# Kernel optimization log

Hardware: AMD Instinct MI355X
Metric: run time of the kernel (lower is better)

## Reference

```python
import jax, jax.numpy as jnp
import numpy as np

H = 128  # hidden width


def _mlp(xy, W0, b0, W1, b1, W2, b2, W3, b3):
    # xy: [..., 2] -> [..., 1], tanh MLP
    h = jnp.tanh(xy @ W0 + b0)
    h = jnp.tanh(h @ W1 + b1)
    h = jnp.tanh(h @ W2 + b2)
    return h @ W3 + b3


def setup_inputs() -> dict:
    key = jax.random.key(0)
    ks = jax.random.split(key, 8)
    n_int, n_bd = 262144, 16384
    inp = {
        "xy_int": jax.random.uniform(ks[0], (n_int, 2), dtype=jnp.float32),
        "f": jax.random.normal(ks[1], (n_int, 1), dtype=jnp.float32),
        "xy_bd": jax.random.uniform(ks[2], (n_bd, 2), dtype=jnp.float32),
        "g": jax.random.normal(ks[3], (n_bd, 1), dtype=jnp.float32),
        # Glorot-ish scaled weights
        "W0": jax.random.normal(ks[4], (2, H), dtype=jnp.float32) / np.sqrt(2.0),
        "b0": jnp.zeros((H,), jnp.float32),
        "W1": jax.random.normal(ks[5], (H, H), dtype=jnp.float32) / np.sqrt(H),
        "b1": jnp.zeros((H,), jnp.float32),
        "W2": jax.random.normal(ks[6], (H, H), dtype=jnp.float32) / np.sqrt(H),
        "b2": jnp.zeros((H,), jnp.float32),
        "W3": jax.random.normal(ks[7], (H, 1), dtype=jnp.float32) / np.sqrt(H),
        "b3": jnp.zeros((1,), jnp.float32),
    }
    return inp


def reference(xy_int, f, xy_bd, g, W0, b0, W1, b1, W2, b2, W3, b3):
    params = (W0, b0, W1, b1, W2, b2, W3, b3)
    n_int = xy_int.shape[0]
    n_bd = xy_bd.shape[0]

    # boundary loss: 0.5/n_bd * ||u(xy_bd) - g||^2
    pred_bd = _mlp(xy_bd, *params)
    diff_bd = pred_bd.reshape(-1) - g.reshape(-1)
    loss_bound = 0.5 / n_bd * jnp.sum(diff_bd * diff_bd)

    # interior PDE residual: u_xx + u_yy (Laplacian) per collocation point
    def u_scalar(p):  # p: [2] -> scalar
        return _mlp(p[None, :], *params)[0, 0]

    def lap_point(p):
        return jnp.trace(jax.hessian(u_scalar)(p))  # 2x2 Hessian trace

    pred_f = jax.vmap(lap_point)(xy_int)  # [n_int]
    diff_f = pred_f.reshape(-1) - f.reshape(-1)
    loss_f = 0.5 / n_int * jnp.sum(diff_f * diff_f)

    return (loss_bound, loss_f)
```

## Files before the change

kernel.cpp:

```cpp
#include <hip/hip_runtime.h>

#define HID 128
#define PTS 32
#define FRAGS_PER_W 2048
#define WS_ELEMS (FRAGS_PER_W * 8)

typedef float v4f  __attribute__((ext_vector_type(4)));
typedef float v16f __attribute__((ext_vector_type(16)));
typedef short s8v  __attribute__((ext_vector_type(8)));

__device__ __forceinline__ unsigned short f2bf(float f) {
    unsigned u = __builtin_bit_cast(unsigned, f);
    u = (u + 0x7FFFu + ((u >> 16) & 1u)) >> 16;
    return (unsigned short)u;
}

#if __has_builtin(__builtin_amdgcn_cvt_pk_bf16_f32)
typedef __bf16 bf16x2 __attribute__((ext_vector_type(2)));
__device__ __forceinline__ unsigned pk2(float f0, float f1) {
    return __builtin_bit_cast(unsigned, __builtin_amdgcn_cvt_pk_bf16_f32(f0, f1));
}
#else
__device__ __forceinline__ unsigned pk2(float f0, float f1) {
    unsigned u0 = __builtin_bit_cast(unsigned, f0);
    unsigned u1 = __builtin_bit_cast(unsigned, f1);
    u0 += 0x7FFFu + ((u0 >> 16) & 1u);
    u1 += 0x7FFFu + ((u1 >> 16) & 1u);
    return __builtin_amdgcn_perm(u1, u0, 0x07060302u);
}
#endif
__device__ __forceinline__ uint2 pk4(const float* f) {
    uint2 h;
    h.x = pk2(f[0], f[1]);
    h.y = pk2(f[2], f[3]);
    return h;
}

__device__ __forceinline__ float fast_tanh(float x) {
#if __has_builtin(__builtin_amdgcn_exp2f)
    float e = __builtin_amdgcn_exp2f(x * 2.885390081777927f);
#else
    float e = __expf(2.0f * x);
#endif
    float r = __builtin_amdgcn_rcpf(e + 1.0f);
    return 1.0f - 2.0f * r;
}

__device__ __forceinline__ void* sb_at(unsigned short* sBh, int row, int colh) {
    return (char*)sBh + (row << 8) + (((colh << 1)) ^ ((row & 15) << 4));
}

__global__ __launch_bounds__(256) void prep_w_kernel(
    const float* __restrict__ W1, const float* __restrict__ W2,
    unsigned short* __restrict__ ws, float* __restrict__ out)
{
    if (blockIdx.x == 0 && threadIdx.x < 2) out[threadIdx.x] = 0.0f;
    const int t = blockIdx.x * 256 + threadIdx.x;
    const int w = t >> 11;
    const int r = t & 2047;
    const int mw = r >> 9;
    const int ks8 = (r >> 6) & 7;
    const int lane = r & 63;
    const int m = mw * 32 + (lane & 31);
    const int kb = ks8 * 16 + (lane >> 5) * 8;
    const float* W = w ? W2 : W1;
    s8v hv;
    #pragma unroll
    for (int i = 0; i < 8; ++i)
        hv[i] = (short)f2bf(W[(kb + i) * HID + m]);
    *(s8v*)&ws[((size_t)w * FRAGS_PER_W + r) * 8] = hv;
}

template <int NC>
__device__ __forceinline__ void run_pinn(
    const float* __restrict__ xy, const float* __restrict__ tgt,
    const float* __restrict__ W0, const float* __restrict__ b0,
    const float* __restrict__ b1, const float* __restrict__ b2,
    const float* __restrict__ W3, const float* __restrict__ b3,
    const unsigned short* __restrict__ ws, float* __restrict__ out_slot,
    float scale, int pbase, unsigned short* sBh, float* sPart)
{
    const int tid  = threadIdx.x;
    const int lane = tid & 63;
    const int mw   = tid >> 6;
    const int l31  = lane & 31;
    const int kh   = lane >> 5;

    s8v wf[8];
    #pragma unroll
    for (int q = 0; q < 8; ++q)
        wf[q] = *(const s8v*)&ws[(size_t)(mw * 512 + q * 64 + lane) * 8];

    {
        const int tj = tid & 31, tp = tid >> 5;
        const int j0 = tj * 4, p0 = tp * 4;
        float wx[4], wy[4], bb[4], m2s2[4];
        #pragma unroll
        for (int jj = 0; jj < 4; ++jj) {
            wx[jj] = W0[j0 + jj];
            wy[jj] = W0[HID + j0 + jj];
            bb[jj] = b0[j0 + jj];
            m2s2[jj] = -2.0f * fmaf(wx[jj], wx[jj], wy[jj] * wy[jj]);
        }
        #pragma unroll
        for (int pp = 0; pp < 4; ++pp) {
            const int p = p0 + pp;
            const float2 t2 = ((const float2*)xy)[pbase + p];
            float chv[NC][4];
            #pragma unroll
            for (int jj = 0; jj < 4; ++jj) {
                float z = fmaf(t2.x, wx[jj], fmaf(t2.y, wy[jj], bb[jj]));
                float a = fast_tanh(z);
                chv[0][jj] = a;
                if (NC == 4) {
                    float t = fmaf(-a, a, 1.0f);
                    chv[1][jj] = t * wx[jj];
                    chv[2][jj] = t * wy[jj];
                    chv[3][jj] = (a * t) * m2s2[jj];
                }
            }
            #pragma unroll
            for (int c = 0; c < NC; ++c)
                *(uint2*)sb_at(sBh, c * 32 + p, j0) = pk4(chv[c]);
        }
    }
    __syncthreads();

    v16f acc[NC];

    #pragma unroll
    for (int L = 0; L < 2; ++L) {
        #pragma unroll
        for (int nt = 0; nt < NC; ++nt) acc[nt] = (v16f)0.0f;

        #pragma unroll
        for (int q = 0; q < 8; ++q) {
            const int koff = q * 16 + kh * 8;
            #pragma unroll
            for (int nt = 0; nt < NC; ++nt) {
                s8v bh = *(const s8v*)sb_at(sBh, nt * 32 + l31, koff);
                acc[nt] = __builtin_amdgcn_mfma_f32_32x32x16_bf16(
                    wf[q], bh, acc[nt], 0, 0, 0);
            }
        }

        if (L == 0) {
            __syncthreads();
            #pragma unroll
            for (int q = 0; q < 8; ++q)
                wf[q] = *(const s8v*)&ws[WS_ELEMS + (size_t)(mw * 512 + q * 64 + lane) * 8];
            #pragma unroll
            for (int g = 0; g < 4; ++g) {
                const int j0g = mw * 32 + 8 * g + 4 * kh;
                const v4f bb = *(const v4f*)&b1[j0g];
                float chv[NC][4];
                #pragma unroll
                for (int r = 0; r < 4; ++r) {
                    float z = acc[0][g * 4 + r] + bb[r];
                    float a = fast_tanh(z);
                    chv[0][r] = a;
                    if (NC == 4) {
                        float t = fmaf(-a, a, 1.0f);
                        float zx = acc[1][g * 4 + r], zy = acc[2][g * 4 + r],
                              zl = acc[3][g * 4 + r];
                        float s2 = fmaf(zx, zx, zy * zy);
                        float u  = fmaf(-(a + a), s2, zl);
                        chv[1][r] = t * zx;
                        chv[2][r] = t * zy;
                        chv[3][r] = t * u;
                    }
                }
                #pragma unroll
                for (int c = 0; c < NC; ++c)
                    *(uint2*)sb_at(sBh, c * 32 + l31, j0g) = pk4(chv[c]);
            }
            __syncthreads();
        }
    }

    {
        float part = 0.0f;
        #pragma unroll
        for (int g = 0; g < 4; ++g) {
            const int j0g = mw * 32 + 8 * g + 4 * kh;
            const v4f bb = *(const v4f*)&b2[j0g];
            const v4f w3 = *(const v4f*)&W3[j0g];
            #pragma unroll
            for (int r = 0; r < 4; ++r) {
                float z = acc[0][g * 4 + r] + bb[r];
                float a = fast_tanh(z);
                float v;
                if (NC == 1) {
                    v = a;
                } else {
                    float t = fmaf(-a, a, 1.0f);
                    float zx = acc[1][g * 4 + r], zy = acc[2][g * 4 + r],
                          zl = acc[3][g * 4 + r];
                    float s2 = fmaf(zx, zx, zy * zy);
                    v = t * fmaf(-(a + a), s2, zl);
                }
                part = fmaf(v, w3[r], part);
            }
        }
        part += __shfl_xor(part, 32, 64);
        if (kh == 0) sPart[mw * 32 + l31] = part;
        __syncthreads();
        if (mw == 0) {
            const int p = l31;
            float pred = (sPart[p] + sPart[32 + p]) + (sPart[64 + p] + sPart[96 + p])
                       + ((NC == 1) ? b3[0] : 0.0f);
            float d = pred - tgt[pbase + p];
            float sq = (kh == 0) ? d * d : 0.0f;
            sq += __shfl_xor(sq, 1, 64);
            sq += __shfl_xor(sq, 2, 64);
            sq += __shfl_xor(sq, 4, 64);
            sq += __shfl_xor(sq, 8, 64);
            sq += __shfl_xor(sq, 16, 64);
            sq += __shfl_xor(sq, 32, 64);
            if (lane == 0) atomicAdd(out_slot, sq * scale);
        }
    }
}

__global__ __launch_bounds__(256, 4) void pinn_mfma_kernel(
    const float* __restrict__ xy_int, const float* __restrict__ f_t,
    const float* __restrict__ xy_bd, const float* __restrict__ g_t,
    const float* __restrict__ W0, const float* __restrict__ b0,
    const float* __restrict__ b1, const float* __restrict__ b2,
    const float* __restrict__ W3, const float* __restrict__ b3,
    const unsigned short* __restrict__ ws, float* __restrict__ out,
    int gi, float scale_int, float scale_bd)
{
    extern __shared__ char smem_raw[];
    unsigned short* sBh = (unsigned short*)smem_raw;
    float* sPart = (float*)(sBh + 4 * 32 * 128);

    const int b = (int)blockIdx.x;
    if (b >= gi)
        run_pinn<1>(xy_bd, g_t, W0, b0, b1, b2, W3, b3, ws,
                    out + 0, scale_bd, (b - gi) * PTS, sBh, sPart);
    else
        run_pinn<4>(xy_int, f_t, W0, b0, b1, b2, W3, b3, ws,
                    out + 1, scale_int, b * PTS, sBh, sPart);
}

extern "C" void kernel_launch(void* const* d_in, const int* in_sizes, int n_in,
                              void* d_out, int out_size, void* d_ws, size_t ws_size,
                              hipStream_t stream) {
    const float* xy_int = (const float*)d_in[0];
    const float* f      = (const float*)d_in[1];
    const float* xy_bd  = (const float*)d_in[2];
    const float* g      = (const float*)d_in[3];
    const float* W0 = (const float*)d_in[4];
    const float* b0 = (const float*)d_in[5];
    const float* W1 = (const float*)d_in[6];
    const float* b1 = (const float*)d_in[7];
    const float* W2 = (const float*)d_in[8];
    const float* b2 = (const float*)d_in[9];
    const float* W3 = (const float*)d_in[10];
    const float* b3 = (const float*)d_in[11];
    float* out = (float*)d_out;
    unsigned short* ws = (unsigned short*)d_ws;

    const int n_int = in_sizes[0] / 2;
    const int n_bd  = in_sizes[2] / 2;

    prep_w_kernel<<<16, 256, 0, stream>>>(W1, W2, ws, out);

    const int smem = 4 * 32 * 128 * 2 + 128 * 4;
    const int gi = n_int / PTS;
    const int gb = n_bd / PTS;

    pinn_mfma_kernel<<<gi + gb, 256, smem, stream>>>(
        xy_int, f, xy_bd, g, W0, b0, b1, b2, W3, b3, ws, out,
        gi, 0.5f / (float)n_int, 0.5f / (float)n_bd);
}
```

Measured before the change: 193.0 us.

## Switch to 16x16x32 MFMA with 8 waves per block and prescaled tanh

Replaces the 32x32x16 bf16 MFMA tiling with 16x16x32 tiles, so each of 8 waves in a 512-thread block owns 16 output rows. This cuts the per-wave weight-fragment and accumulator register footprint so more waves can be resident. The weight pre-packing layout and the cross-wave reduction are reworked to match. The tanh input is also prescaled by 2/ln2 and folded into the weights and biases, saving a multiply per activation. The risks are extra LDS B-fragment reads per MFMA and more block-level synchronisation across 8 waves.

Measured after the change: 192.2 us. Within noise of the previous version (-0.4%).

```diff
diff --git a/kernel.cpp b/kernel.cpp
--- a/kernel.cpp
+++ b/kernel.cpp
@@ -4,9 +4,9 @@
 #define PTS 32
 #define FRAGS_PER_W 2048
 #define WS_ELEMS (FRAGS_PER_W * 8)
+#define TANH_K 2.885390081777927f
 
 typedef float v4f  __attribute__((ext_vector_type(4)));
-typedef float v16f __attribute__((ext_vector_type(16)));
 typedef short s8v  __attribute__((ext_vector_type(8)));
 
 __device__ __forceinline__ unsigned short f2bf(float f) {
@@ -36,14 +36,14 @@
     return h;
 }
 
-__device__ __forceinline__ float fast_tanh(float x) {
+__device__ __forceinline__ float tanh_pre(float xp) {
 #if __has_builtin(__builtin_amdgcn_exp2f)
-    float e = __builtin_amdgcn_exp2f(x * 2.885390081777927f);
+    float e = __builtin_amdgcn_exp2f(xp);
 #else
-    float e = __expf(2.0f * x);
+    float e = __expf(xp * 0.6931471805599453f);
 #endif
     float r = __builtin_amdgcn_rcpf(e + 1.0f);
-    return 1.0f - 2.0f * r;
+    return fmaf(-2.0f, r, 1.0f);
 }
 
 __device__ __forceinline__ void* sb_at(unsigned short* sBh, int row, int colh) {
@@ -58,11 +58,11 @@
     const int t = blockIdx.x * 256 + threadIdx.x;
     const int w = t >> 11;
     const int r = t & 2047;
-    const int mw = r >> 9;
-    const int ks8 = (r >> 6) & 7;
+    const int mw = r >> 8;
+    const int s  = (r >> 6) & 3;
     const int lane = r & 63;
-    const int m = mw * 32 + (lane & 31);
-    const int kb = ks8 * 16 + (lane >> 5) * 8;
+    const int m = mw * 16 + (lane & 15);
+    const int kb = s * 32 + (lane >> 4) * 8;
     const float* W = w ? W2 : W1;
     s8v hv;
     #pragma unroll
@@ -83,34 +83,32 @@
     const int tid  = threadIdx.x;
     const int lane = tid & 63;
     const int mw   = tid >> 6;
-    const int l31  = lane & 31;
-    const int kh   = lane >> 5;
-
-    s8v wf[8];
-    #pragma unroll
-    for (int q = 0; q < 8; ++q)
-        wf[q] = *(const s8v*)&ws[(size_t)(mw * 512 + q * 64 + lane) * 8];
+    const int l15  = lane & 15;
+    const int kg   = lane >> 4;
 
     {
         const int tj = tid & 31, tp = tid >> 5;
-        const int j0 = tj * 4, p0 = tp * 4;
-        float wx[4], wy[4], bb[4], m2s2[4];
+        const int j0 = tj * 4, p0 = tp * 2;
+        float wx[4], wy[4], m2s2[4], wxK[4], wyK[4], bbK[4];
         #pragma unroll
         for (int jj = 0; jj < 4; ++jj) {
             wx[jj] = W0[j0 + jj];
             wy[jj] = W0[HID + j0 + jj];
-            bb[jj] = b0[j0 + jj];
+            float bb = b0[j0 + jj];
+            wxK[jj] = TANH_K * wx[jj];
+            wyK[jj] = TANH_K * wy[jj];
+            bbK[jj] = TANH_K * bb;
             m2s2[jj] = -2.0f * fmaf(wx[jj], wx[jj], wy[jj] * wy[jj]);
         }
         #pragma unroll
-        for (int pp = 0; pp < 4; ++pp) {
+        for (int pp = 0; pp < 2; ++pp) {
             const int p = p0 + pp;
             const float2 t2 = ((const float2*)xy)[pbase + p];
             float chv[NC][4];
             #pragma unroll
             for (int jj = 0; jj < 4; ++jj) {
-                float z = fmaf(t2.x, wx[jj], fmaf(t2.y, wy[jj], bb[jj]));
-                float a = fast_tanh(z);
+                float xp = fmaf(t2.x, wxK[jj], fmaf(t2.y, wyK[jj], bbK[jj]));
+                float a = tanh_pre(xp);
                 chv[0][jj] = a;
                 if (NC == 4) {
                     float t = fmaf(-a, a, 1.0f);
@@ -124,45 +122,56 @@
                 *(uint2*)sb_at(sBh, c * 32 + p, j0) = pk4(chv[c]);
         }
     }
+
+    s8v wf[4];
+    #pragma unroll
+    for (int s = 0; s < 4; ++s)
+        wf[s] = *(const s8v*)&ws[(size_t)((mw * 4 + s) * 64 + lane) * 8];
+
     __syncthreads();
 
-    v16f acc[NC];
+    v4f acc[NC][2];
 
     #pragma unroll
     for (int L = 0; L < 2; ++L) {
         #pragma unroll
-        for (int nt = 0; nt < NC; ++nt) acc[nt] = (v16f)0.0f;
-
-        #pragma unroll
-        for (int q = 0; q < 8; ++q) {
-            const int koff = q * 16 + kh * 8;
-            #pragma unroll
-            for (int nt = 0; nt < NC; ++nt) {
-                s8v bh = *(const s8v*)sb_at(sBh, nt * 32 + l31, koff);
-                acc[nt] = __builtin_amdgcn_mfma_f32_32x32x16_bf16(
-                    wf[q], bh, acc[nt], 0, 0, 0);
+        for (int c = 0; c < NC; ++c)
+            #pragma unroll
+            for (int ns = 0; ns < 2; ++ns) acc[c][ns] = (v4f)0.0f;
+
+        #pragma unroll
+        for (int s = 0; s < 4; ++s) {
+            const int colh = s * 32 + kg * 8;
+            #pragma unroll
+            for (int c = 0; c < NC; ++c) {
+                #pragma unroll
+                for (int ns = 0; ns < 2; ++ns) {
+                    s8v bh = *(const s8v*)sb_at(sBh, c * 32 + ns * 16 + l15, colh);
+                    acc[c][ns] = __builtin_amdgcn_mfma_f32_16x16x32_bf16(
+                        wf[s], bh, acc[c][ns], 0, 0, 0);
+                }
             }
         }
 
         if (L == 0) {
             __syncthreads();
             #pragma unroll
-            for (int q = 0; q < 8; ++q)
-                wf[q] = *(const s8v*)&ws[WS_ELEMS + (size_t)(mw * 512 + q * 64 + lane) * 8];
-            #pragma unroll
-            for (int g = 0; g < 4; ++g) {
-                const int j0g = mw * 32 + 8 * g + 4 * kh;
-                const v4f bb = *(const v4f*)&b1[j0g];
+            for (int s = 0; s < 4; ++s)
+                wf[s] = *(const s8v*)&ws[WS_ELEMS + (size_t)((mw * 4 + s) * 64 + lane) * 8];
+            const int jb = mw * 16 + kg * 4;
+            const v4f bb = *(const v4f*)&b1[jb];
+            const v4f bbK = TANH_K * bb;
+            #pragma unroll
+            for (int ns = 0; ns < 2; ++ns) {
                 float chv[NC][4];
                 #pragma unroll
                 for (int r = 0; r < 4; ++r) {
-                    float z = acc[0][g * 4 + r] + bb[r];
-                    float a = fast_tanh(z);
+                    float a = tanh_pre(fmaf(acc[0][ns][r], TANH_K, bbK[r]));
                     chv[0][r] = a;
                     if (NC == 4) {
                         float t = fmaf(-a, a, 1.0f);
-                        float zx = acc[1][g * 4 + r], zy = acc[2][g * 4 + r],
-                              zl = acc[3][g * 4 + r];
+                        float zx = acc[1][ns][r], zy = acc[2][ns][r],
+                              zl = acc[3][ns][r];
                         float s2 = fmaf(zx, zx, zy * zy);
                         float u  = fmaf(-(a + a), s2, zl);
                         chv[1][r] = t * zx;
@@ -172,45 +181,54 @@
                 }
                 #pragma unroll
                 for (int c = 0; c < NC; ++c)
-                    *(uint2*)sb_at(sBh, c * 32 + l31, j0g) = pk4(chv[c]);
+                    *(uint2*)sb_at(sBh, c * 32 + ns * 16 + l15, jb) = pk4(chv[c]);
             }
             __syncthreads();
         }
     }
 
     {
-        float part = 0.0f;
-        #pragma unroll
-        for (int g = 0; g < 4; ++g) {
-            const int j0g = mw * 32 + 8 * g + 4 * kh;
-            const v4f bb = *(const v4f*)&b2[j0g];
-            const v4f w3 = *(const v4f*)&W3[j0g];
+        const int jb = mw * 16 + kg * 4;
+        const v4f bb = *(const v4f*)&b2[jb];
+        const v4f bbK = TANH_K * bb;
+        const v4f w3 = *(const v4f*)&W3[jb];
+        float part[2];
+        #pragma unroll
+        for (int ns = 0; ns < 2; ++ns) {
+            part[ns] = 0.0f;
             #pragma unroll
             for (int r = 0; r < 4; ++r) {
-                float z = acc[0][g * 4 + r] + bb[r];
-                float a = fast_tanh(z);
+                float a = tanh_pre(fmaf(acc[0][ns][r], TANH_K, bbK[r]));
                 float v;
                 if (NC == 1) {
                     v = a;
                 } else {
                     float t = fmaf(-a, a, 1.0f);
-                    float zx = acc[1][g * 4 + r], zy = acc[2][g * 4 + r],
-                          zl = acc[3][g * 4 + r];
+                    float zx = acc[1][ns][r], zy = acc[2][ns][r],
+                          zl = acc[3][ns][r];
                     float s2 = fmaf(zx, zx, zy * zy);
                     v = t * fmaf(-(a + a), s2, zl);
                 }
-                part = fmaf(v, w3[r], part);
-            }
-        }
-        part += __shfl_xor(part, 32, 64);
-        if (kh == 0) sPart[mw * 32 + l31] = part;
+                part[ns] = fmaf(v, w3[r], part[ns]);
+            }
+            part[ns] += __shfl_xor(part[ns], 16, 64);
+            part[ns] += __shfl_xor(part[ns], 32, 64);
+        }
+        if (lane < 16) {
+            sPart[mw * 32 + lane]      = part[0];
+            sPart[mw * 32 + 16 + lane] = part[1];
+        }
         __syncthreads();
         if (mw == 0) {
-            const int p = l31;
-            float pred = (sPart[p] + sPart[32 + p]) + (sPart[64 + p] + sPart[96 + p])
-                       + ((NC == 1) ? b3[0] : 0.0f);
+            const int p = lane & 31;
+            const int h = lane >> 5;
+            const int w0 = h * 4;
+            float sum = (sPart[w0 * 32 + p] + sPart[(w0 + 1) * 32 + p])
+                      + (sPart[(w0 + 2) * 32 + p] + sPart[(w0 + 3) * 32 + p]);
+            sum += __shfl_xor(sum, 32, 64);
+            float pred = sum + ((NC == 1) ? b3[0] : 0.0f);
             float d = pred - tgt[pbase + p];
-            float sq = (kh == 0) ? d * d : 0.0f;
+            float sq = (h == 0) ? d * d : 0.0f;
             sq += __shfl_xor(sq, 1, 64);
             sq += __shfl_xor(sq, 2, 64);
             sq += __shfl_xor(sq, 4, 64);
@@ -222,7 +240,7 @@
     }
 }
 
-__global__ __launch_bounds__(256, 4) void pinn_mfma_kernel(
+__global__ __launch_bounds__(512, 6) void pinn_mfma_kernel(
     const float* __restrict__ xy_int, const float* __restrict__ f_t,
     const float* __restrict__ xy_bd, const float* __restrict__ g_t,
     const float* __restrict__ W0, const float* __restrict__ b0,
@@ -267,11 +285,11 @@
 
     prep_w_kernel<<<16, 256, 0, stream>>>(W1, W2, ws, out);
 
-    const int smem = 4 * 32 * 128 * 2 + 128 * 4;
+    const int smem = 4 * 32 * 128 * 2 + 8 * 32 * 4;
     const int gi = n_int / PTS;
     const int gb = n_bd / PTS;
 
-    pinn_mfma_kernel<<<gi + gb, 256, smem, stream>>>(
+    pinn_mfma_kernel<<<gi + gb, 512, smem, stream>>>(
         xy_int, f, xy_bd, g, W0, b0, b1, b2, W3, b3, ws, out,
         gi, 0.5f / (float)n_int, 0.5f / (float)n_bd);
 }
```
